# Kernel tuning notes

Hardware: AMD Instinct MI355X
Metric: run time of the kernel (lower is better)

Reference implementation:

```python
import jax, jax.numpy as jnp
import numpy as np

B, NPG, F, DEG = 512, 512, 255, 32   # graphs, nodes-per-graph, feat dim, avg degree
N = B * NPG
E = N * DEG
RATIO = 0.5
K = int(np.ceil(RATIO * NPG))        # nodes kept per graph (static)


def setup_inputs() -> dict:
    key = jax.random.key(0)
    k1, k2, k3, k4, k5 = jax.random.split(key, 5)
    out = jax.random.normal(k1, (N, F), jnp.float32)
    z = jax.random.randint(k2, (N,), 0, 101)  # z == 100 marks virtual nodes
    # random edges strictly within each graph (block-contiguous node ids)
    local = jax.random.randint(k3, (2, B, NPG * DEG), 0, NPG)
    offs = (jnp.arange(B) * NPG)[None, :, None]
    edge_index = (local + offs).reshape(2, E)
    batch = jnp.repeat(jnp.arange(B), NPG)
    W = jax.random.normal(k4, (F + 1, 1), jnp.float32) * (1.0 / np.sqrt(F + 1))
    b = jnp.zeros((1,), jnp.float32)
    edge_attr = jax.random.normal(k5, (E, 1), jnp.float32)  # carried but unused by SAGPool scoring
    return dict(out=out, z=z, edge_index=edge_index, batch=batch, W=W, b=b,
                edge_attr=edge_attr)


def gcn_score(x, edge_index, W, b):
    """GCNConv(F+1 -> 1) with self-loops and symmetric normalization."""
    n = x.shape[0]
    h = (x @ W)[:, 0]  # [N] since out_channels == 1
    row, col = edge_index[0], edge_index[1]
    loop = jnp.arange(n)
    row = jnp.concatenate([row, loop])
    col = jnp.concatenate([col, loop])
    deg = jax.ops.segment_sum(jnp.ones_like(col, x.dtype), col, num_segments=n)
    dinv = jnp.where(deg > 0, jax.lax.rsqrt(deg), 0.0)
    norm = dinv[row] * dinv[col]  # deg^-1/2 * deg^-1/2 per edge
    agg = jax.ops.segment_sum(norm * h[row], col, num_segments=n)
    return agg + b[0]


def reference(out, z, edge_index, batch, W, b, edge_attr):
    # concat real/virtual bit
    real = (z != 100).astype(out.dtype)[:, None]
    x = jnp.concatenate([out, real], axis=-1)          # [N, F+1]
    # SAGPooling: score nodes, tanh nonlinearity
    score = jnp.tanh(gcn_score(x, edge_index, W, b))   # [N]
    # per-graph top-k (uniform graph size -> static-shape top_k)
    sv, si = jax.lax.top_k(score.reshape(B, NPG), K)   # [B, K]
    perm = (si + (jnp.arange(B) * NPG)[:, None]).reshape(-1)  # global node ids
    xp = x[perm] * sv.reshape(-1)[:, None]             # gated selected nodes [B*K, F+1]
    # global_mean_pool over pooled batch (k nodes per graph)
    return xp.reshape(B, K, F + 1).mean(axis=1)        # [B, F+1]
```

## Files before the change

kernel.cpp:

```cpp
#include <hip/hip_runtime.h>
#include <math.h>

#define NPG     512
#define B_GR    512
#define FDIM    255
#define DEG     32
#define EPG     (NPG * DEG)
#define N_NODES (B_GR * NPG)
#define E_TOT   (N_NODES * DEG)
#define K_KEEP  256

#define NPB   32
#define FPB   (NPB * FDIM)
#define F4PB  (FPB / 4)

__global__ __launch_bounds__(512) void k_proj(const float* __restrict__ feat,
                                              const int*   __restrict__ z,
                                              const float* __restrict__ W,
                                              float*       __restrict__ h) {
    __shared__ float4 stage4[F4PB];
    __shared__ float  Wl[256];
    __shared__ float  realw[NPB];

    const int tid   = threadIdx.x;
    const int nbase = blockIdx.x * NPB;

    if (tid < 256) Wl[tid] = W[tid];
    if (tid < NPB) realw[tid] = (z[nbase + tid] != 100) ? W[FDIM] : 0.f;

    const float4* src = (const float4*)(feat + (size_t)nbase * FDIM);
#pragma unroll
    for (int it = 0; it < 4; ++it) {
        const int idx = it * 512 + tid;
        if (idx < F4PB) stage4[idx] = src[idx];
    }
    __syncthreads();

    const float* stage = (const float*)stage4;
    const int wave = tid >> 6;
    const int lane = tid & 63;
#pragma unroll
    for (int k = 0; k < 4; ++k) {
        const int node = wave * 4 + k;
        const float* row = stage + node * FDIM;
        float acc = (lane == 0) ? realw[node] : 0.f;
        acc = fmaf(row[lane],       Wl[lane],       acc);
        acc = fmaf(row[lane + 64],  Wl[lane + 64],  acc);
        acc = fmaf(row[lane + 128], Wl[lane + 128], acc);
        if (lane < 63)
            acc = fmaf(row[lane + 192], Wl[lane + 192], acc);
#pragma unroll
        for (int off = 32; off; off >>= 1)
            acc += __shfl_down(acc, off, 64);
        if (lane == 0) h[nbase + node] = acc;
    }
}

__global__ __launch_bounds__(1024) void k_score(const float* __restrict__ feat,
                                                const int*   __restrict__ z,
                                                const int*   __restrict__ ei,
                                                const float* __restrict__ bias,
                                                const float* __restrict__ h,
                                                float*       __restrict__ outp) {
    __shared__ float h_l[NPG];
    __shared__ float dinv_l[NPG];
    __shared__ float agg[NPG];
    __shared__ float score[NPG];
    __shared__ float realb[NPG];
    __shared__ int   deg[NPG];
    __shared__ int   rank2[2][NPG];
    __shared__ int   selidx[K_KEEP];
    __shared__ float selsc[K_KEEP];
    __shared__ float red[3][256];
    __shared__ int   cnt;

    const int g     = blockIdx.x;
    const int tid   = threadIdx.x;
    const int nbase = g * NPG;

    if (tid < NPG) {
        h_l[tid] = h[nbase + tid];
        deg[tid] = 1;
        agg[tid] = 0.f;
    } else {
        const int t = tid - NPG;
        realb[t] = (z[nbase + t] != 100) ? 1.f : 0.f;
    }
    if (tid == 0) cnt = 0;
    __syncthreads();

    const int4* colp4 = (const int4*)(ei + (size_t)E_TOT + (size_t)g * EPG);
    const int4* rowp4 = (const int4*)(ei + (size_t)g * EPG);

#pragma unroll
    for (int it = 0; it < 4; ++it) {
        const int4 c4 = colp4[it * 1024 + tid];
        atomicAdd(&deg[c4.x - nbase], 1);
        atomicAdd(&deg[c4.y - nbase], 1);
        atomicAdd(&deg[c4.z - nbase], 1);
        atomicAdd(&deg[c4.w - nbase], 1);
    }
    __syncthreads();

    if (tid < NPG)
        dinv_l[tid] = (float)(1.0 / sqrt((double)deg[tid]));
    __syncthreads();

#pragma unroll
    for (int it = 0; it < 4; ++it) {
        const int4 r4 = rowp4[it * 1024 + tid];
        const int4 c4 = colp4[it * 1024 + tid];
        int r, c;
        r = r4.x - nbase; c = c4.x - nbase; atomicAdd(&agg[c], dinv_l[r] * dinv_l[c] * h_l[r]);
        r = r4.y - nbase; c = c4.y - nbase; atomicAdd(&agg[c], dinv_l[r] * dinv_l[c] * h_l[r]);
        r = r4.z - nbase; c = c4.z - nbase; atomicAdd(&agg[c], dinv_l[r] * dinv_l[c] * h_l[r]);
        r = r4.w - nbase; c = c4.w - nbase; atomicAdd(&agg[c], dinv_l[r] * dinv_l[c] * h_l[r]);
    }
    __syncthreads();

    if (tid < NPG)
        score[tid] = tanhf(agg[tid] + dinv_l[tid] * dinv_l[tid] * h_l[tid] + bias[0]);
    __syncthreads();

    {
        const int node = tid & (NPG - 1);
        const int half = tid >> 9;
        const float sc = score[node];
        const int j0   = half * 256;
        int part = 0;
        for (int i = 0; i < 256; ++i) {
            const int j = j0 + i;
            const float sj = score[j];
            part += (sj > sc) || (sj == sc && j < node);
        }
        rank2[half][node] = part;
    }
    __syncthreads();

    if (tid < NPG) {
        const int rank = rank2[0][tid] + rank2[1][tid];
        if (rank < K_KEEP) {
            const int slot = atomicAdd(&cnt, 1);
            selidx[slot] = tid;
            selsc[slot]  = score[tid];
        }
    }
    __syncthreads();

    const int f = tid & 255;
    const int q = tid >> 8;
    float acc = 0.f;
    if (f < FDIM) {
        const float* fb = feat + (size_t)nbase * FDIM + f;
#pragma unroll 8
        for (int s = q; s < K_KEEP; s += 4)
            acc = fmaf(selsc[s], fb[(size_t)selidx[s] * FDIM], acc);
    } else {
#pragma unroll 8
        for (int s = q; s < K_KEEP; s += 4)
            acc = fmaf(selsc[s], realb[selidx[s]], acc);
    }
    if (q) red[q - 1][f] = acc;
    __syncthreads();
    if (q == 0)
        outp[(size_t)g * 256 + f] =
            (acc + red[0][f] + red[1][f] + red[2][f]) * (1.f / K_KEEP);
}

extern "C" void kernel_launch(void* const* d_in, const int* in_sizes, int n_in,
                              void* d_out, int out_size, void* d_ws, size_t ws_size,
                              hipStream_t stream) {
    const float* feat = (const float*)d_in[0];
    const int*   z    = (const int*)  d_in[1];
    const int*   ei   = (const int*)  d_in[2];
    const float* W    = (const float*)d_in[4];
    const float* bias = (const float*)d_in[5];
    float* outp = (float*)d_out;
    float* h    = (float*)d_ws;

    k_proj<<<N_NODES / NPB, 512, 0, stream>>>(feat, z, W, h);
    k_score<<<B_GR, 1024, 0, stream>>>(feat, z, ei, bias, h, outp);
}
```

Before: 130.3 us.

## Fuse projection into per-graph scoring kernel and cache column indices in LDS

Merges the node projection kernel into the per-graph scoring kernel, so each block computes h for its 512 nodes by staging feature chunks in shared memory. This removes the h round-trip through global memory and one kernel launch. It also caches column indices as 16-bit values in the reused staging buffer, so the aggregation pass does not reload them from global memory. In exchange, projection parallelism drops to 512 blocks with a serial chunk loop and more barriers, and shared memory use per block grows.

```diff
diff --git a/kernel.cpp b/kernel.cpp
--- a/kernel.cpp
+++ b/kernel.cpp
@@ -10,58 +10,18 @@
 #define E_TOT   (N_NODES * DEG)
 #define K_KEEP  256
 
-#define NPB   32
-#define FPB   (NPB * FDIM)
-#define F4PB  (FPB / 4)
+#define CH_NODES 32
+#define CH_F4    ((CH_NODES * FDIM) / 4)
+#define NCHUNK   (NPG / CH_NODES)
 
-__global__ __launch_bounds__(512) void k_proj(const float* __restrict__ feat,
-                                              const int*   __restrict__ z,
-                                              const float* __restrict__ W,
-                                              float*       __restrict__ h) {
-    __shared__ float4 stage4[F4PB];
-    __shared__ float  Wl[256];
-    __shared__ float  realw[NPB];
-
-    const int tid   = threadIdx.x;
-    const int nbase = blockIdx.x * NPB;
-
-    if (tid < 256) Wl[tid] = W[tid];
-    if (tid < NPB) realw[tid] = (z[nbase + tid] != 100) ? W[FDIM] : 0.f;
-
-    const float4* src = (const float4*)(feat + (size_t)nbase * FDIM);
-#pragma unroll
-    for (int it = 0; it < 4; ++it) {
-        const int idx = it * 512 + tid;
-        if (idx < F4PB) stage4[idx] = src[idx];
-    }
-    __syncthreads();
-
-    const float* stage = (const float*)stage4;
-    const int wave = tid >> 6;
-    const int lane = tid & 63;
-#pragma unroll
-    for (int k = 0; k < 4; ++k) {
-        const int node = wave * 4 + k;
-        const float* row = stage + node * FDIM;
-        float acc = (lane == 0) ? realw[node] : 0.f;
-        acc = fmaf(row[lane],       Wl[lane],       acc);
-        acc = fmaf(row[lane + 64],  Wl[lane + 64],  acc);
-        acc = fmaf(row[lane + 128], Wl[lane + 128], acc);
-        if (lane < 63)
-            acc = fmaf(row[lane + 192], Wl[lane + 192], acc);
-#pragma unroll
-        for (int off = 32; off; off >>= 1)
-            acc += __shfl_down(acc, off, 64);
-        if (lane == 0) h[nbase + node] = acc;
-    }
-}
-
-__global__ __launch_bounds__(1024) void k_score(const float* __restrict__ feat,
+__global__ __launch_bounds__(1024) void k_fused(const float* __restrict__ feat,
                                                 const int*   __restrict__ z,
                                                 const int*   __restrict__ ei,
+                                                const float* __restrict__ W,
                                                 const float* __restrict__ bias,
-                                                const float* __restrict__ h,
                                                 float*       __restrict__ outp) {
+    __shared__ __align__(16) char stagebuf[32768];
+    __shared__ float Wl[256];
     __shared__ float h_l[NPG];
     __shared__ float dinv_l[NPG];
     __shared__ float agg[NPG];
@@ -78,58 +38,98 @@
     const int tid   = threadIdx.x;
     const int nbase = g * NPG;
 
+    if (tid < 256) Wl[tid] = W[tid];
     if (tid < NPG) {
-        h_l[tid] = h[nbase + tid];
-        deg[tid] = 1;
-        agg[tid] = 0.f;
-    } else {
-        const int t = tid - NPG;
-        realb[t] = (z[nbase + t] != 100) ? 1.f : 0.f;
+        realb[tid] = (z[nbase + tid] != 100) ? 1.f : 0.f;
+        deg[tid]   = 1;
+        agg[tid]   = 0.f;
     }
     if (tid == 0) cnt = 0;
     __syncthreads();
 
-    const int4* colp4 = (const int4*)(ei + (size_t)E_TOT + (size_t)g * EPG);
-    const int4* rowp4 = (const int4*)(ei + (size_t)g * EPG);
+    {
+        float4*      stage4 = (float4*)stagebuf;
+        const float* stage  = (const float*)stagebuf;
+        const int    wave   = tid >> 6;
+        const int    lane   = tid & 63;
+        const float4* src   = (const float4*)(feat + (size_t)nbase * FDIM);
+
+        for (int ch = 0; ch < NCHUNK; ++ch) {
+            stage4[tid] = src[ch * CH_F4 + tid];
+            const int idx2 = 1024 + tid;
+            if (idx2 < CH_F4) stage4[idx2] = src[ch * CH_F4 + idx2];
+            __syncthreads();
+#pragma unroll
+            for (int k = 0; k < 2; ++k) {
+                const int node = wave * 2 + k;
+                const float* row = stage + node * FDIM;
+                float acc = (lane == 0) ? realb[ch * CH_NODES + node] * Wl[FDIM] : 0.f;
+                acc = fmaf(row[lane],       Wl[lane],       acc);
+                acc = fmaf(row[lane + 64],  Wl[lane + 64],  acc);
+                acc = fmaf(row[lane + 128], Wl[lane + 128], acc);
+                if (lane < 63)
+                    acc = fmaf(row[lane + 192], Wl[lane + 192], acc);
+#pragma unroll
+                for (int off = 32; off; off >>= 1)
+                    acc += __shfl_down(acc, off, 64);
+                if (lane == 0) h_l[ch * CH_NODES + node] = acc;
+            }
+            __syncthreads();
+        }
+    }
+
+    {
+        ushort4*    cc4   = (ushort4*)stagebuf;
+        const int4* colp4 = (const int4*)(ei + (size_t)E_TOT + (size_t)g * EPG);
+        const int4* rowp4 = (const int4*)(ei + (size_t)g * EPG);
 
 #pragma unroll
-    for (int it = 0; it < 4; ++it) {
-        const int4 c4 = colp4[it * 1024 + tid];
-        atomicAdd(&deg[c4.x - nbase], 1);
-        atomicAdd(&deg[c4.y - nbase], 1);
-        atomicAdd(&deg[c4.z - nbase], 1);
-        atomicAdd(&deg[c4.w - nbase], 1);
-    }
-    __syncthreads();
+        for (int it = 0; it < 4; ++it) {
+            const int  idx = it * 1024 + tid;
+            const int4 c4  = colp4[idx];
+            ushort4 u;
+            u.x = (unsigned short)(c4.x - nbase);
+            u.y = (unsigned short)(c4.y - nbase);
+            u.z = (unsigned short)(c4.z - nbase);
+            u.w = (unsigned short)(c4.w - nbase);
+            cc4[idx] = u;
+            atomicAdd(&deg[u.x], 1);
+            atomicAdd(&deg[u.y], 1);
+            atomicAdd(&deg[u.z], 1);
+            atomicAdd(&deg[u.w], 1);
+        }
+        __syncthreads();
 
-    if (tid < NPG)
-        dinv_l[tid] = (float)(1.0 / sqrt((double)deg[tid]));
-    __syncthreads();
+        if (tid < NPG)
+            dinv_l[tid] = (float)(1.0 / sqrt((double)deg[tid]));
+        __syncthreads();
 
 #pragma unroll
-    for (int it = 0; it < 4; ++it) {
-        const int4 r4 = rowp4[it * 1024 + tid];
-        const int4 c4 = colp4[it * 1024 + tid];
-        int r, c;
-        r = r4.x - nbase; c = c4.x - nbase; atomicAdd(&agg[c], dinv_l[r] * dinv_l[c] * h_l[r]);
-        r = r4.y - nbase; c = c4.y - nbase; atomicAdd(&agg[c], dinv_l[r] * dinv_l[c] * h_l[r]);
-        r = r4.z - nbase; c = c4.z - nbase; atomicAdd(&agg[c], dinv_l[r] * dinv_l[c] * h_l[r]);
-        r = r4.w - nbase; c = c4.w - nbase; atomicAdd(&agg[c], dinv_l[r] * dinv_l[c] * h_l[r]);
+        for (int it = 0; it < 4; ++it) {
+            const int     idx = it * 1024 + tid;
+            const int4    r4  = rowp4[idx];
+            const ushort4 u   = cc4[idx];
+            int r;
+            r = r4.x - nbase; atomicAdd(&agg[u.x], dinv_l[r] * dinv_l[u.x] * h_l[r]);
+            r = r4.y - nbase; atomicAdd(&agg[u.y], dinv_l[r] * dinv_l[u.y] * h_l[r]);
+            r = r4.z - nbase; atomicAdd(&agg[u.z], dinv_l[r] * dinv_l[u.z] * h_l[r]);
+            r = r4.w - nbase; atomicAdd(&agg[u.w], dinv_l[r] * dinv_l[u.w] * h_l[r]);
+        }
+        __syncthreads();
     }
-    __syncthreads();
 
     if (tid < NPG)
         score[tid] = tanhf(agg[tid] + dinv_l[tid] * dinv_l[tid] * h_l[tid] + bias[0]);
     __syncthreads();
 
     {
-        const int node = tid & (NPG - 1);
-        const int half = tid >> 9;
-        const float sc = score[node];
-        const int j0   = half * 256;
+        const int   node = tid & (NPG - 1);
+        const int   half = tid >> 9;
+        const float sc   = score[node];
+        const int   j0   = half * 256;
         int part = 0;
         for (int i = 0; i < 256; ++i) {
-            const int j = j0 + i;
+            const int   j  = j0 + i;
             const float sj = score[j];
             part += (sj > sc) || (sj == sc && j < node);
         }
@@ -147,24 +147,26 @@
     }
     __syncthreads();
 
-    const int f = tid & 255;
-    const int q = tid >> 8;
-    float acc = 0.f;
-    if (f < FDIM) {
-        const float* fb = feat + (size_t)nbase * FDIM + f;
+    {
+        const int f = tid & 255;
+        const int q = tid >> 8;
+        float acc = 0.f;
+        if (f < FDIM) {
+            const float* fb = feat + (size_t)nbase * FDIM + f;
 #pragma unroll 8
-        for (int s = q; s < K_KEEP; s += 4)
-            acc = fmaf(selsc[s], fb[(size_t)selidx[s] * FDIM], acc);
-    } else {
+            for (int s = q; s < K_KEEP; s += 4)
+                acc = fmaf(selsc[s], fb[(size_t)selidx[s] * FDIM], acc);
+        } else {
 #pragma unroll 8
-        for (int s = q; s < K_KEEP; s += 4)
-            acc = fmaf(selsc[s], realb[selidx[s]], acc);
+            for (int s = q; s < K_KEEP; s += 4)
+                acc = fmaf(selsc[s], realb[selidx[s]], acc);
+        }
+        if (q) red[q - 1][f] = acc;
+        __syncthreads();
+        if (q == 0)
+            outp[(size_t)g * 256 + f] =
+                (acc + red[0][f] + red[1][f] + red[2][f]) * (1.f / K_KEEP);
     }
-    if (q) red[q - 1][f] = acc;
-    __syncthreads();
-    if (q == 0)
-        outp[(size_t)g * 256 + f] =
-            (acc + red[0][f] + red[1][f] + red[2][f]) * (1.f / K_KEEP);
 }
 
 extern "C" void kernel_launch(void* const* d_in, const int* in_sizes, int n_in,
@@ -176,8 +178,6 @@
     const float* W    = (const float*)d_in[4];
     const float* bias = (const float*)d_in[5];
     float* outp = (float*)d_out;
-    float* h    = (float*)d_ws;
 
-    k_proj<<<N_NODES / NPB, 512, 0, stream>>>(feat, z, W, h);
-    k_score<<<B_GR, 1024, 0, stream>>>(feat, z, ei, bias, h, outp);
+    k_fused<<<B_GR, 1024, 0, stream>>>(feat, z, ei, W, bias, outp);
 }
```

New measurement: 128.7 us. About the same (-1.2%).
